# Kernel optimization log

Hardware: AMD Instinct MI355X
Metric: run time of the kernel (lower is better)

## Reference

```python
import jax, jax.numpy as jnp
import numpy as np

D = 4096  # domain size of every variable X, Y, Z, W


def setup_inputs() -> dict:
    key = jax.random.key(0)
    ks = jax.random.split(key, 7)
    theta0 = jax.random.normal(ks[0], (D, D), dtype=jnp.float32)  # clique (X, Y)
    theta1 = jax.random.normal(ks[1], (D, D), dtype=jnp.float32)  # clique (Y, Z)
    theta2 = jax.random.normal(ks[2], (D, D), dtype=jnp.float32)  # clique (Z, W)
    ops = {f"op{i}": jax.random.randint(ks[3 + i], (2, D), 0, D, dtype=jnp.int32)
           for i in range(4)}
    return {"theta0": theta0, "theta1": theta1, "theta2": theta2, **ops}


def _remap(proc, op, dom):
    # torch: zeros(dom).index_add_(0, op[1], proc[op[0]])
    return jnp.zeros((dom,), proc.dtype).at[op[1]].add(proc[op[0]])


def reference(theta0, theta1, theta2, op0, op1, op2, op3):
    dom = theta0.shape[0]
    # m0: clique0 -> clique1 (forward): sum over X (dim 0), remap Y, broadcast over Z
    m0 = _remap(jnp.sum(theta0, axis=0), op0, dom)
    theta1 = theta1 + m0[:, None]          # reshape_dims [True, False]
    # m1: clique1 -> clique2 (forward): sum over Y (dim 0), remap Z
    m1 = _remap(jnp.sum(theta1, axis=0), op1, dom)
    theta2 = theta2 + m1[:, None]
    # m2: clique2 -> clique1 (backward): sum over W (dim 1), subtract stored fwd msg m1
    m2 = _remap(jnp.sum(theta2, axis=1) - m1, op2, dom)
    theta1 = theta1 + m2[None, :]          # reshape_dims [False, True]
    # m3: clique1 -> clique0 (backward): sum over Z (dim 1), subtract stored fwd msg m0
    m3 = _remap(jnp.sum(theta1, axis=1) - m0, op3, dom)
    theta0 = theta0 + m3[None, :]
    return (theta0, theta1, theta2)
```

## Files before the change

### kernel.cpp

```cpp
#include <hip/hip_runtime.h>

#define D 4096

typedef float fx4 __attribute__((ext_vector_type(4)));

#define CS0 0
#define CS1 D
#define RS1 (2 * D)
#define RS2 (3 * D)
#define M0O (4 * D)
#define M1O (5 * D)
#define M2O (6 * D)
#define M3O (7 * D)
#define S2S (8 * D)

__global__ void __launch_bounds__(256) colsum_kernel(
        const float* __restrict__ t0, const float* __restrict__ t1,
        float* __restrict__ ws) {
    int b = blockIdx.x;
    const float* A = (b < 256) ? t0 : t1;
    float* out = ws + ((b < 256) ? CS0 : CS1);
    int lb = b & 255;
    int c4 = (lb & 3) * 256 + threadIdx.x;
    int r0 = (lb >> 2) * 64;
    const fx4* A4 = (const fx4*)A;
    fx4 s = (fx4){0.f, 0.f, 0.f, 0.f};
    #pragma unroll 8
    for (int r = 0; r < 64; ++r)
        s += A4[(size_t)(r0 + r) * (D / 4) + c4];
    atomicAdd(&out[c4 * 4 + 0], s.x);
    atomicAdd(&out[c4 * 4 + 1], s.y);
    atomicAdd(&out[c4 * 4 + 2], s.z);
    atomicAdd(&out[c4 * 4 + 3], s.w);
}


__device__ __forceinline__ float block_sum_1024(float v, float* red) {
    #pragma unroll
    for (int o = 32; o > 0; o >>= 1) v += __shfl_down(v, o);
    int lane = threadIdx.x & 63, wid = threadIdx.x >> 6;
    if (lane == 0) red[wid] = v;
    __syncthreads();
    if (threadIdx.x == 0) {
        float t = 0.f;
        #pragma unroll
        for (int w = 0; w < 16; ++w) t += red[w];
        red[0] = t;
    }
    __syncthreads();
    float r = red[0];
    __syncthreads();
    return r;
}

__global__ void __launch_bounds__(1024) msgsA_kernel(
        float* __restrict__ ws, const int* __restrict__ op0,
        const int* __restrict__ op1) {
    __shared__ float m0[D], m1[D];
    __shared__ float red[16];
    int tid = threadIdx.x;

    int s0[4], d0[4], s1[4], d1[4];
    #pragma unroll
    for (int k = 0; k < 4; ++k) {
        int i = tid + k * 1024;
        s0[k] = op0[i]; d0[k] = op0[D + i];
        s1[k] = op1[i]; d1[k] = op1[D + i];
    }
    float g0[4], g1[4];
    #pragma unroll
    for (int k = 0; k < 4; ++k) {
        g0[k] = ws[CS0 + s0[k]];
        g1[k] = ws[CS1 + s1[k]];
    }
    #pragma unroll
    for (int k = 0; k < 4; ++k) {
        int i = tid + k * 1024;
        m0[i] = 0.f; m1[i] = 0.f;
    }
    __syncthreads();
    #pragma unroll
    for (int k = 0; k < 4; ++k) atomicAdd(&m0[d0[k]], g0[k]);
    __syncthreads();
    float p = 0.f;
    #pragma unroll
    for (int k = 0; k < 4; ++k) p += m0[tid + k * 1024];
    float S0 = block_sum_1024(p, red);
    #pragma unroll
    for (int k = 0; k < 4; ++k) atomicAdd(&m1[d1[k]], g1[k] + S0);
    __syncthreads();
    #pragma unroll
    for (int k = 0; k < 4; ++k) {
        int i = tid + k * 1024;
        ws[M0O + i] = m0[i];
        ws[M1O + i] = m1[i];
    }
}

__global__ void __launch_bounds__(1024) msgsB_kernel(
        float* __restrict__ ws, const int* __restrict__ op2) {
    __shared__ float m2[D];
    __shared__ float red[16];
    int tid = threadIdx.x;

    int s2[4], d2[4];
    #pragma unroll
    for (int k = 0; k < 4; ++k) {
        int i = tid + k * 1024;
        s2[k] = op2[i]; d2[k] = op2[D + i];
    }
    float g2[4];
    #pragma unroll
    for (int k = 0; k < 4; ++k)
        g2[k] = ws[RS2 + s2[k]] + 4095.0f * ws[M1O + s2[k]];
    #pragma unroll
    for (int k = 0; k < 4; ++k) m2[tid + k * 1024] = 0.f;
    __syncthreads();
    #pragma unroll
    for (int k = 0; k < 4; ++k) atomicAdd(&m2[d2[k]], g2[k]);
    __syncthreads();
    float p = 0.f;
    #pragma unroll
    for (int k = 0; k < 4; ++k) p += m2[tid + k * 1024];
    float S2 = block_sum_1024(p, red);
    #pragma unroll
    for (int k = 0; k < 4; ++k) {
        int i = tid + k * 1024;
        ws[M2O + i] = m2[i];
    }
    if (tid == 0) ws[S2S] = S2;
}

__global__ void __launch_bounds__(1024) msgsC_kernel(
        float* __restrict__ ws, const int* __restrict__ op3) {
    __shared__ float m3[D];
    int tid = threadIdx.x;

    int s3[4], d3[4];
    #pragma unroll
    for (int k = 0; k < 4; ++k) {
        int i = tid + k * 1024;
        s3[k] = op3[i]; d3[k] = op3[D + i];
    }
    float S2 = ws[S2S];
    float g3[4];
    #pragma unroll
    for (int k = 0; k < 4; ++k)
        g3[k] = ws[RS1 + s3[k]] + 4095.0f * ws[M0O + s3[k]] + S2;
    #pragma unroll
    for (int k = 0; k < 4; ++k) m3[tid + k * 1024] = 0.f;
    __syncthreads();
    #pragma unroll
    for (int k = 0; k < 4; ++k) atomicAdd(&m3[d3[k]], g3[k]);
    __syncthreads();
    #pragma unroll
    for (int k = 0; k < 4; ++k) {
        int i = tid + k * 1024;
        ws[M3O + i] = m3[i];
    }
}


__device__ __forceinline__ void row_reduce_store(float s, float* dst) {
    __shared__ float red[4];
    #pragma unroll
    for (int o = 32; o > 0; o >>= 1) s += __shfl_down(s, o);
    int lane = threadIdx.x & 63, wid = threadIdx.x >> 6;
    if (lane == 0) red[wid] = s;
    __syncthreads();
    if (threadIdx.x == 0) *dst = (red[0] + red[1]) + (red[2] + red[3]);
}

__global__ void __launch_bounds__(256) applyT2_kernel(
        const float* __restrict__ t2, float* __restrict__ ws,
        float* __restrict__ out2) {
    int row = blockIdx.x;
    size_t base = (size_t)row * D;
    const fx4* src = (const fx4*)(t2 + base);
    fx4* dst = (fx4*)(out2 + base);
    float rr = ws[M1O + row];

    fx4 v[4];
    float s = 0.f;
    #pragma unroll
    for (int k = 0; k < 4; ++k) {
        v[k] = src[threadIdx.x + 256 * k];
        s += (v[k].x + v[k].y) + (v[k].z + v[k].w);
    }
    #pragma unroll
    for (int k = 0; k < 4; ++k)
        __builtin_nontemporal_store(v[k] + rr, &dst[threadIdx.x + 256 * k]);
    row_reduce_store(s, ws + RS2 + row);
}

__global__ void __launch_bounds__(256) applyT1_kernel(
        const float* __restrict__ t1, float* __restrict__ ws,
        float* __restrict__ out1) {
    int row = blockIdx.x;
    size_t base = (size_t)row * D;
    const fx4* src = (const fx4*)(t1 + base);
    const fx4* c4 = (const fx4*)(ws + M2O);
    fx4* dst = (fx4*)(out1 + base);
    float rr = ws[M0O + row];

    fx4 v[4], c[4];
    float s = 0.f;
    #pragma unroll
    for (int k = 0; k < 4; ++k) {
        v[k] = src[threadIdx.x + 256 * k];
        c[k] = c4[threadIdx.x + 256 * k];
        s += (v[k].x + v[k].y) + (v[k].z + v[k].w);
    }
    #pragma unroll
    for (int k = 0; k < 4; ++k)
        __builtin_nontemporal_store(v[k] + c[k] + rr,
                                    &dst[threadIdx.x + 256 * k]);
    row_reduce_store(s, ws + RS1 + row);
}

__global__ void __launch_bounds__(256) applyT0_kernel(
        const float* __restrict__ t0, const float* __restrict__ ws,
        float* __restrict__ out0) {
    int row = blockIdx.x;
    size_t base = (size_t)row * D;
    const fx4* src = (const fx4*)(t0 + base);
    const fx4* c4 = (const fx4*)(ws + M3O);
    fx4* dst = (fx4*)(out0 + base);

    #pragma unroll
    for (int k = 0; k < 4; ++k) {
        fx4 r = src[threadIdx.x + 256 * k] + c4[threadIdx.x + 256 * k];
        __builtin_nontemporal_store(r, &dst[threadIdx.x + 256 * k]);
    }
}

extern "C" void kernel_launch(void* const* d_in, const int* in_sizes, int n_in,
                              void* d_out, int out_size, void* d_ws, size_t ws_size,
                              hipStream_t stream) {
    const float* t0 = (const float*)d_in[0];
    const float* t1 = (const float*)d_in[1];
    const float* t2 = (const float*)d_in[2];
    const int* op0 = (const int*)d_in[3];
    const int* op1 = (const int*)d_in[4];
    const int* op2 = (const int*)d_in[5];
    const int* op3 = (const int*)d_in[6];
    float* out = (float*)d_out;
    float* ws = (float*)d_ws;

    hipMemsetAsync(ws, 0, 2 * D * sizeof(float), stream);

    colsum_kernel<<<512, 256, 0, stream>>>(t0, t1, ws);
    msgsA_kernel<<<1, 1024, 0, stream>>>(ws, op0, op1);
    applyT2_kernel<<<D, 256, 0, stream>>>(t2, ws, out + 2 * (size_t)D * D);
    msgsB_kernel<<<1, 1024, 0, stream>>>(ws, op2);
    applyT1_kernel<<<D, 256, 0, stream>>>(t1, ws, out + 1 * (size_t)D * D);
    msgsC_kernel<<<1, 1024, 0, stream>>>(ws, op3);
    applyT0_kernel<<<D, 256, 0, stream>>>(t0, ws, out + 0 * (size_t)D * D);
}
```

Before: 135.0 us.

## Fuse single-block message kernels into preceding kernels via last-block-done counters

Folds each single-block message computation (msgsA/B/C) into the tail of the preceding grid-wide kernel. A global atomic counter elects the last finishing block, which then performs the scatter-add remap. This removes three kernel launches and their serialization gaps. In exchange, the tail message work runs on 256 threads instead of 1024, each block adds an atomic counter increment, and the row sums now use atomicAdd into a zeroed workspace whose memset grows.

```diff
diff --git a/kernel.cpp b/kernel.cpp
--- a/kernel.cpp
+++ b/kernel.cpp
@@ -8,214 +8,225 @@
 #define CS1 D
 #define RS1 (2 * D)
 #define RS2 (3 * D)
-#define M0O (4 * D)
-#define M1O (5 * D)
-#define M2O (6 * D)
-#define M3O (7 * D)
-#define S2S (8 * D)
-
-__global__ void __launch_bounds__(256) colsum_kernel(
-        const float* __restrict__ t0, const float* __restrict__ t1,
-        float* __restrict__ ws) {
-    int b = blockIdx.x;
-    const float* A = (b < 256) ? t0 : t1;
-    float* out = ws + ((b < 256) ? CS0 : CS1);
-    int lb = b & 255;
-    int c4 = (lb & 3) * 256 + threadIdx.x;
-    int r0 = (lb >> 2) * 64;
-    const fx4* A4 = (const fx4*)A;
-    fx4 s = (fx4){0.f, 0.f, 0.f, 0.f};
-    #pragma unroll 8
-    for (int r = 0; r < 64; ++r)
-        s += A4[(size_t)(r0 + r) * (D / 4) + c4];
-    atomicAdd(&out[c4 * 4 + 0], s.x);
-    atomicAdd(&out[c4 * 4 + 1], s.y);
-    atomicAdd(&out[c4 * 4 + 2], s.z);
-    atomicAdd(&out[c4 * 4 + 3], s.w);
-}
-
-
-__device__ __forceinline__ float block_sum_1024(float v, float* red) {
+#define CNTA (4 * D)
+#define CNTB (4 * D + 1)
+#define CNTC (4 * D + 2)
+#define M0O (4 * D + 16)
+#define M1O (5 * D + 16)
+#define M2O (6 * D + 16)
+#define M3O (7 * D + 16)
+#define S2S (8 * D + 16)
+
+__device__ __forceinline__ float block_sum_256(float v, float* red) {
     #pragma unroll
     for (int o = 32; o > 0; o >>= 1) v += __shfl_down(v, o);
     int lane = threadIdx.x & 63, wid = threadIdx.x >> 6;
     if (lane == 0) red[wid] = v;
     __syncthreads();
-    if (threadIdx.x == 0) {
-        float t = 0.f;
-        #pragma unroll
-        for (int w = 0; w < 16; ++w) t += red[w];
-        red[0] = t;
-    }
+    if (threadIdx.x == 0) red[0] = (red[0] + red[1]) + (red[2] + red[3]);
     __syncthreads();
     float r = red[0];
     __syncthreads();
     return r;
 }
 
-__global__ void __launch_bounds__(1024) msgsA_kernel(
-        float* __restrict__ ws, const int* __restrict__ op0,
-        const int* __restrict__ op1) {
+__global__ void __launch_bounds__(256) colsum_msgsA_kernel(
+        const float* __restrict__ t0, const float* __restrict__ t1,
+        float* __restrict__ ws,
+        const int* __restrict__ op0, const int* __restrict__ op1) {
+    int b = blockIdx.x, tid = threadIdx.x;
+    {
+        const float* A = (b < 256) ? t0 : t1;
+        float* outp = ws + ((b < 256) ? CS0 : CS1);
+        int lb = b & 255;
+        int c4 = (lb & 3) * 256 + tid;
+        int r0 = (lb >> 2) * 64;
+        const fx4* A4 = (const fx4*)A;
+        fx4 s = (fx4){0.f, 0.f, 0.f, 0.f};
+        #pragma unroll 8
+        for (int r = 0; r < 64; ++r)
+            s += A4[(size_t)(r0 + r) * (D / 4) + c4];
+        atomicAdd(&outp[c4 * 4 + 0], s.x);
+        atomicAdd(&outp[c4 * 4 + 1], s.y);
+        atomicAdd(&outp[c4 * 4 + 2], s.z);
+        atomicAdd(&outp[c4 * 4 + 3], s.w);
+    }
+    __syncthreads();
+    __shared__ unsigned int lastflag;
+    if (tid == 0)
+        lastflag = (atomicAdd((unsigned int*)(ws + CNTA), 1u) == 511u);
+    __syncthreads();
+    if (!lastflag) return;
+    __threadfence();
+
     __shared__ float m0[D], m1[D];
-    __shared__ float red[16];
-    int tid = threadIdx.x;
-
-    int s0[4], d0[4], s1[4], d1[4];
-    #pragma unroll
-    for (int k = 0; k < 4; ++k) {
-        int i = tid + k * 1024;
-        s0[k] = op0[i]; d0[k] = op0[D + i];
-        s1[k] = op1[i]; d1[k] = op1[D + i];
-    }
-    float g0[4], g1[4];
-    #pragma unroll
-    for (int k = 0; k < 4; ++k) {
-        g0[k] = ws[CS0 + s0[k]];
-        g1[k] = ws[CS1 + s1[k]];
-    }
-    #pragma unroll
-    for (int k = 0; k < 4; ++k) {
-        int i = tid + k * 1024;
-        m0[i] = 0.f; m1[i] = 0.f;
-    }
-    __syncthreads();
-    #pragma unroll
-    for (int k = 0; k < 4; ++k) atomicAdd(&m0[d0[k]], g0[k]);
+    __shared__ float red[4];
+    #pragma unroll
+    for (int k = 0; k < 16; ++k) {
+        m0[tid + 256 * k] = 0.f; m1[tid + 256 * k] = 0.f;
+    }
+    __syncthreads();
+    #pragma unroll
+    for (int c = 0; c < 2; ++c) {
+        int sx[8], dx[8]; float g[8];
+        #pragma unroll
+        for (int j = 0; j < 8; ++j) {
+            int i = tid + (c * 8 + j) * 256;
+            sx[j] = op0[i]; dx[j] = op0[D + i];
+        }
+        #pragma unroll
+        for (int j = 0; j < 8; ++j) g[j] = ws[CS0 + sx[j]];
+        #pragma unroll
+        for (int j = 0; j < 8; ++j) atomicAdd(&m0[dx[j]], g[j]);
+    }
     __syncthreads();
     float p = 0.f;
     #pragma unroll
-    for (int k = 0; k < 4; ++k) p += m0[tid + k * 1024];
-    float S0 = block_sum_1024(p, red);
-    #pragma unroll
-    for (int k = 0; k < 4; ++k) atomicAdd(&m1[d1[k]], g1[k] + S0);
-    __syncthreads();
-    #pragma unroll
-    for (int k = 0; k < 4; ++k) {
-        int i = tid + k * 1024;
-        ws[M0O + i] = m0[i];
-        ws[M1O + i] = m1[i];
-    }
-}
-
-__global__ void __launch_bounds__(1024) msgsB_kernel(
-        float* __restrict__ ws, const int* __restrict__ op2) {
+    for (int k = 0; k < 16; ++k) p += m0[tid + 256 * k];
+    float S0 = block_sum_256(p, red);
+    #pragma unroll
+    for (int c = 0; c < 2; ++c) {
+        int sx[8], dx[8]; float g[8];
+        #pragma unroll
+        for (int j = 0; j < 8; ++j) {
+            int i = tid + (c * 8 + j) * 256;
+            sx[j] = op1[i]; dx[j] = op1[D + i];
+        }
+        #pragma unroll
+        for (int j = 0; j < 8; ++j) g[j] = ws[CS1 + sx[j]];
+        #pragma unroll
+        for (int j = 0; j < 8; ++j) atomicAdd(&m1[dx[j]], g[j] + S0);
+    }
+    __syncthreads();
+    #pragma unroll
+    for (int k = 0; k < 16; ++k) {
+        ws[M0O + tid + 256 * k] = m0[tid + 256 * k];
+        ws[M1O + tid + 256 * k] = m1[tid + 256 * k];
+    }
+}
+
+__global__ void __launch_bounds__(256) applyT2_msgsB_kernel(
+        const float* __restrict__ t2, float* __restrict__ ws,
+        float* __restrict__ out2, const int* __restrict__ op2) {
+    int row = blockIdx.x, tid = threadIdx.x;
+    __shared__ float red[4];
+    {
+        size_t base = (size_t)row * D;
+        const fx4* src = (const fx4*)(t2 + base);
+        fx4* dst = (fx4*)(out2 + base);
+        float rr = ws[M1O + row];
+        fx4 v[4]; float s = 0.f;
+        #pragma unroll
+        for (int k = 0; k < 4; ++k) {
+            v[k] = src[tid + 256 * k];
+            s += (v[k].x + v[k].y) + (v[k].z + v[k].w);
+        }
+        #pragma unroll
+        for (int k = 0; k < 4; ++k)
+            __builtin_nontemporal_store(v[k] + rr, &dst[tid + 256 * k]);
+        #pragma unroll
+        for (int o = 32; o > 0; o >>= 1) s += __shfl_down(s, o);
+        int lane = tid & 63, wid = tid >> 6;
+        if (lane == 0) red[wid] = s;
+        __syncthreads();
+        if (tid == 0)
+            atomicAdd(&ws[RS2 + row], (red[0] + red[1]) + (red[2] + red[3]));
+    }
+    __syncthreads();
+    __shared__ unsigned int lastflag;
+    if (tid == 0)
+        lastflag = (atomicAdd((unsigned int*)(ws + CNTB), 1u) == (unsigned)(D - 1));
+    __syncthreads();
+    if (!lastflag) return;
+    __threadfence();
+
     __shared__ float m2[D];
-    __shared__ float red[16];
-    int tid = threadIdx.x;
-
-    int s2[4], d2[4];
-    #pragma unroll
-    for (int k = 0; k < 4; ++k) {
-        int i = tid + k * 1024;
-        s2[k] = op2[i]; d2[k] = op2[D + i];
-    }
-    float g2[4];
-    #pragma unroll
-    for (int k = 0; k < 4; ++k)
-        g2[k] = ws[RS2 + s2[k]] + 4095.0f * ws[M1O + s2[k]];
-    #pragma unroll
-    for (int k = 0; k < 4; ++k) m2[tid + k * 1024] = 0.f;
-    __syncthreads();
-    #pragma unroll
-    for (int k = 0; k < 4; ++k) atomicAdd(&m2[d2[k]], g2[k]);
+    #pragma unroll
+    for (int k = 0; k < 16; ++k) m2[tid + 256 * k] = 0.f;
+    __syncthreads();
+    #pragma unroll
+    for (int c = 0; c < 2; ++c) {
+        int sx[8], dx[8]; float g[8];
+        #pragma unroll
+        for (int j = 0; j < 8; ++j) {
+            int i = tid + (c * 8 + j) * 256;
+            sx[j] = op2[i]; dx[j] = op2[D + i];
+        }
+        #pragma unroll
+        for (int j = 0; j < 8; ++j)
+            g[j] = ws[RS2 + sx[j]] + 4095.0f * ws[M1O + sx[j]];
+        #pragma unroll
+        for (int j = 0; j < 8; ++j) atomicAdd(&m2[dx[j]], g[j]);
+    }
     __syncthreads();
     float p = 0.f;
     #pragma unroll
-    for (int k = 0; k < 4; ++k) p += m2[tid + k * 1024];
-    float S2 = block_sum_1024(p, red);
-    #pragma unroll
-    for (int k = 0; k < 4; ++k) {
-        int i = tid + k * 1024;
-        ws[M2O + i] = m2[i];
-    }
+    for (int k = 0; k < 16; ++k) p += m2[tid + 256 * k];
+    float S2 = block_sum_256(p, red);
+    #pragma unroll
+    for (int k = 0; k < 16; ++k) ws[M2O + tid + 256 * k] = m2[tid + 256 * k];
     if (tid == 0) ws[S2S] = S2;
 }
 
-__global__ void __launch_bounds__(1024) msgsC_kernel(
-        float* __restrict__ ws, const int* __restrict__ op3) {
+__global__ void __launch_bounds__(256) applyT1_msgsC_kernel(
+        const float* __restrict__ t1, float* __restrict__ ws,
+        float* __restrict__ out1, const int* __restrict__ op3) {
+    int row = blockIdx.x, tid = threadIdx.x;
+    __shared__ float red[4];
+    {
+        size_t base = (size_t)row * D;
+        const fx4* src = (const fx4*)(t1 + base);
+        const fx4* c4 = (const fx4*)(ws + M2O);
+        fx4* dst = (fx4*)(out1 + base);
+        float rr = ws[M0O + row];
+        fx4 v[4], c[4]; float s = 0.f;
+        #pragma unroll
+        for (int k = 0; k < 4; ++k) {
+            v[k] = src[tid + 256 * k];
+            c[k] = c4[tid + 256 * k];
+            s += (v[k].x + v[k].y) + (v[k].z + v[k].w);
+        }
+        #pragma unroll
+        for (int k = 0; k < 4; ++k)
+            __builtin_nontemporal_store(v[k] + c[k] + rr, &dst[tid + 256 * k]);
+        #pragma unroll
+        for (int o = 32; o > 0; o >>= 1) s += __shfl_down(s, o);
+        int lane = tid & 63, wid = tid >> 6;
+        if (lane == 0) red[wid] = s;
+        __syncthreads();
+        if (tid == 0)
+            atomicAdd(&ws[RS1 + row], (red[0] + red[1]) + (red[2] + red[3]));
+    }
+    __syncthreads();
+    __shared__ unsigned int lastflag;
+    if (tid == 0)
+        lastflag = (atomicAdd((unsigned int*)(ws + CNTC), 1u) == (unsigned)(D - 1));
+    __syncthreads();
+    if (!lastflag) return;
+    __threadfence();
+
     __shared__ float m3[D];
-    int tid = threadIdx.x;
-
-    int s3[4], d3[4];
-    #pragma unroll
-    for (int k = 0; k < 4; ++k) {
-        int i = tid + k * 1024;
-        s3[k] = op3[i]; d3[k] = op3[D + i];
-    }
     float S2 = ws[S2S];
-    float g3[4];
-    #pragma unroll
-    for (int k = 0; k < 4; ++k)
-        g3[k] = ws[RS1 + s3[k]] + 4095.0f * ws[M0O + s3[k]] + S2;
-    #pragma unroll
-    for (int k = 0; k < 4; ++k) m3[tid + k * 1024] = 0.f;
-    __syncthreads();
-    #pragma unroll
-    for (int k = 0; k < 4; ++k) atomicAdd(&m3[d3[k]], g3[k]);
-    __syncthreads();
-    #pragma unroll
-    for (int k = 0; k < 4; ++k) {
-        int i = tid + k * 1024;
-        ws[M3O + i] = m3[i];
-    }
-}
-
-
-__device__ __forceinline__ void row_reduce_store(float s, float* dst) {
-    __shared__ float red[4];
-    #pragma unroll
-    for (int o = 32; o > 0; o >>= 1) s += __shfl_down(s, o);
-    int lane = threadIdx.x & 63, wid = threadIdx.x >> 6;
-    if (lane == 0) red[wid] = s;
-    __syncthreads();
-    if (threadIdx.x == 0) *dst = (red[0] + red[1]) + (red[2] + red[3]);
-}
-
-__global__ void __launch_bounds__(256) applyT2_kernel(
-        const float* __restrict__ t2, float* __restrict__ ws,
-        float* __restrict__ out2) {
-    int row = blockIdx.x;
-    size_t base = (size_t)row * D;
-    const fx4* src = (const fx4*)(t2 + base);
-    fx4* dst = (fx4*)(out2 + base);
-    float rr = ws[M1O + row];
-
-    fx4 v[4];
-    float s = 0.f;
-    #pragma unroll
-    for (int k = 0; k < 4; ++k) {
-        v[k] = src[threadIdx.x + 256 * k];
-        s += (v[k].x + v[k].y) + (v[k].z + v[k].w);
-    }
-    #pragma unroll
-    for (int k = 0; k < 4; ++k)
-        __builtin_nontemporal_store(v[k] + rr, &dst[threadIdx.x + 256 * k]);
-    row_reduce_store(s, ws + RS2 + row);
-}
-
-__global__ void __launch_bounds__(256) applyT1_kernel(
-        const float* __restrict__ t1, float* __restrict__ ws,
-        float* __restrict__ out1) {
-    int row = blockIdx.x;
-    size_t base = (size_t)row * D;
-    const fx4* src = (const fx4*)(t1 + base);
-    const fx4* c4 = (const fx4*)(ws + M2O);
-    fx4* dst = (fx4*)(out1 + base);
-    float rr = ws[M0O + row];
-
-    fx4 v[4], c[4];
-    float s = 0.f;
-    #pragma unroll
-    for (int k = 0; k < 4; ++k) {
-        v[k] = src[threadIdx.x + 256 * k];
-        c[k] = c4[threadIdx.x + 256 * k];
-        s += (v[k].x + v[k].y) + (v[k].z + v[k].w);
-    }
-    #pragma unroll
-    for (int k = 0; k < 4; ++k)
-        __builtin_nontemporal_store(v[k] + c[k] + rr,
-                                    &dst[threadIdx.x + 256 * k]);
-    row_reduce_store(s, ws + RS1 + row);
+    #pragma unroll
+    for (int k = 0; k < 16; ++k) m3[tid + 256 * k] = 0.f;
+    __syncthreads();
+    #pragma unroll
+    for (int c = 0; c < 2; ++c) {
+        int sx[8], dx[8]; float g[8];
+        #pragma unroll
+        for (int j = 0; j < 8; ++j) {
+            int i = tid + (c * 8 + j) * 256;
+            sx[j] = op3[i]; dx[j] = op3[D + i];
+        }
+        #pragma unroll
+        for (int j = 0; j < 8; ++j)
+            g[j] = ws[RS1 + sx[j]] + 4095.0f * ws[M0O + sx[j]] + S2;
+        #pragma unroll
+        for (int j = 0; j < 8; ++j) atomicAdd(&m3[dx[j]], g[j]);
+    }
+    __syncthreads();
+    #pragma unroll
+    for (int k = 0; k < 16; ++k) ws[M3O + tid + 256 * k] = m3[tid + 256 * k];
 }
 
 __global__ void __launch_bounds__(256) applyT0_kernel(
@@ -226,7 +237,6 @@
     const fx4* src = (const fx4*)(t0 + base);
     const fx4* c4 = (const fx4*)(ws + M3O);
     fx4* dst = (fx4*)(out0 + base);
-
     #pragma unroll
     for (int k = 0; k < 4; ++k) {
         fx4 r = src[threadIdx.x + 256 * k] + c4[threadIdx.x + 256 * k];
@@ -247,13 +257,10 @@
     float* out = (float*)d_out;
     float* ws = (float*)d_ws;
 
-    hipMemsetAsync(ws, 0, 2 * D * sizeof(float), stream);
-
-    colsum_kernel<<<512, 256, 0, stream>>>(t0, t1, ws);
-    msgsA_kernel<<<1, 1024, 0, stream>>>(ws, op0, op1);
-    applyT2_kernel<<<D, 256, 0, stream>>>(t2, ws, out + 2 * (size_t)D * D);
-    msgsB_kernel<<<1, 1024, 0, stream>>>(ws, op2);
-    applyT1_kernel<<<D, 256, 0, stream>>>(t1, ws, out + 1 * (size_t)D * D);
-    msgsC_kernel<<<1, 1024, 0, stream>>>(ws, op3);
+    hipMemsetAsync(ws, 0, (4 * D + 16) * sizeof(float), stream);
+
+    colsum_msgsA_kernel<<<512, 256, 0, stream>>>(t0, t1, ws, op0, op1);
+    applyT2_msgsB_kernel<<<D, 256, 0, stream>>>(t2, ws, out + 2 * (size_t)D * D, op2);
+    applyT1_msgsC_kernel<<<D, 256, 0, stream>>>(t1, ws, out + 1 * (size_t)D * D, op3);
     applyT0_kernel<<<D, 256, 0, stream>>>(t0, ws, out + 0 * (size_t)D * D);
 }
```

Measured after the change: 191.0 us. 1.42x slower.

## Precompute theta1 row sums in reduce pass and merge backward message kernels

Applied to the files above, without the earlier changes.

Row sums of the original theta1 are now computed in the first reduction kernel, using 1024 extra blocks with one wave per row, instead of in applyT1. The m2 and m3 message computations are merged into one single-block kernel, which removes one launch and one serial dependency. applyT1 becomes a pure elementwise add with no reduction. The cost is a second read of theta1 in the first pass, about 64 MB of extra traffic, in exchange for one fewer serialized single-block kernel launch.

```diff
diff --git a/kernel.cpp b/kernel.cpp
--- a/kernel.cpp
+++ b/kernel.cpp
@@ -12,26 +12,41 @@
 #define M1O (5 * D)
 #define M2O (6 * D)
 #define M3O (7 * D)
-#define S2S (8 * D)
-
-__global__ void __launch_bounds__(256) colsum_kernel(
+
+__global__ void __launch_bounds__(256) reduce_kernel(
         const float* __restrict__ t0, const float* __restrict__ t1,
         float* __restrict__ ws) {
     int b = blockIdx.x;
-    const float* A = (b < 256) ? t0 : t1;
-    float* out = ws + ((b < 256) ? CS0 : CS1);
-    int lb = b & 255;
-    int c4 = (lb & 3) * 256 + threadIdx.x;
-    int r0 = (lb >> 2) * 64;
-    const fx4* A4 = (const fx4*)A;
-    fx4 s = (fx4){0.f, 0.f, 0.f, 0.f};
-    #pragma unroll 8
-    for (int r = 0; r < 64; ++r)
-        s += A4[(size_t)(r0 + r) * (D / 4) + c4];
-    atomicAdd(&out[c4 * 4 + 0], s.x);
-    atomicAdd(&out[c4 * 4 + 1], s.y);
-    atomicAdd(&out[c4 * 4 + 2], s.z);
-    atomicAdd(&out[c4 * 4 + 3], s.w);
+    if (b < 512) {
+        const float* A = (b < 256) ? t0 : t1;
+        float* out = ws + ((b < 256) ? CS0 : CS1);
+        int lb = b & 255;
+        int c4 = (lb & 3) * 256 + threadIdx.x;
+        int r0 = (lb >> 2) * 64;
+        const fx4* A4 = (const fx4*)A;
+        fx4 s = (fx4){0.f, 0.f, 0.f, 0.f};
+        #pragma unroll 8
+        for (int r = 0; r < 64; ++r)
+            s += A4[(size_t)(r0 + r) * (D / 4) + c4];
+        atomicAdd(&out[c4 * 4 + 0], s.x);
+        atomicAdd(&out[c4 * 4 + 1], s.y);
+        atomicAdd(&out[c4 * 4 + 2], s.z);
+        atomicAdd(&out[c4 * 4 + 3], s.w);
+    } else {
+        int lb = b - 512;
+        int wid = threadIdx.x >> 6, lane = threadIdx.x & 63;
+        int row = lb * 4 + wid;
+        const fx4* R = (const fx4*)(t1 + (size_t)row * D);
+        float s = 0.f;
+        #pragma unroll
+        for (int j = 0; j < 16; ++j) {
+            fx4 v = R[lane + 64 * j];
+            s += (v.x + v.y) + (v.z + v.w);
+        }
+        #pragma unroll
+        for (int o = 32; o > 0; o >>= 1) s += __shfl_down(s, o);
+        if (lane == 0) ws[RS1 + row] = s;
+    }
 }
 
 
@@ -97,24 +112,31 @@
     }
 }
 
-__global__ void __launch_bounds__(1024) msgsB_kernel(
-        float* __restrict__ ws, const int* __restrict__ op2) {
-    __shared__ float m2[D];
+__global__ void __launch_bounds__(1024) msgsBC_kernel(
+        float* __restrict__ ws, const int* __restrict__ op2,
+        const int* __restrict__ op3) {
+    __shared__ float m2[D], m3[D];
     __shared__ float red[16];
     int tid = threadIdx.x;
 
-    int s2[4], d2[4];
+    int s2[4], d2[4], s3[4], d3[4];
     #pragma unroll
     for (int k = 0; k < 4; ++k) {
         int i = tid + k * 1024;
         s2[k] = op2[i]; d2[k] = op2[D + i];
-    }
-    float g2[4];
-    #pragma unroll
-    for (int k = 0; k < 4; ++k)
-        g2[k] = ws[RS2 + s2[k]] + 4095.0f * ws[M1O + s2[k]];
-    #pragma unroll
-    for (int k = 0; k < 4; ++k) m2[tid + k * 1024] = 0.f;
+        s3[k] = op3[i]; d3[k] = op3[D + i];
+    }
+    float g2[4], g3p[4];
+    #pragma unroll
+    for (int k = 0; k < 4; ++k) {
+        g2[k]  = ws[RS2 + s2[k]] + 4095.0f * ws[M1O + s2[k]];
+        g3p[k] = ws[RS1 + s3[k]] + 4095.0f * ws[M0O + s3[k]];
+    }
+    #pragma unroll
+    for (int k = 0; k < 4; ++k) {
+        int i = tid + k * 1024;
+        m2[i] = 0.f; m3[i] = 0.f;
+    }
     __syncthreads();
     #pragma unroll
     for (int k = 0; k < 4; ++k) atomicAdd(&m2[d2[k]], g2[k]);
@@ -124,38 +146,12 @@
     for (int k = 0; k < 4; ++k) p += m2[tid + k * 1024];
     float S2 = block_sum_1024(p, red);
     #pragma unroll
+    for (int k = 0; k < 4; ++k) atomicAdd(&m3[d3[k]], g3p[k] + S2);
+    __syncthreads();
+    #pragma unroll
     for (int k = 0; k < 4; ++k) {
         int i = tid + k * 1024;
         ws[M2O + i] = m2[i];
-    }
-    if (tid == 0) ws[S2S] = S2;
-}
-
-__global__ void __launch_bounds__(1024) msgsC_kernel(
-        float* __restrict__ ws, const int* __restrict__ op3) {
-    __shared__ float m3[D];
-    int tid = threadIdx.x;
-
-    int s3[4], d3[4];
-    #pragma unroll
-    for (int k = 0; k < 4; ++k) {
-        int i = tid + k * 1024;
-        s3[k] = op3[i]; d3[k] = op3[D + i];
-    }
-    float S2 = ws[S2S];
-    float g3[4];
-    #pragma unroll
-    for (int k = 0; k < 4; ++k)
-        g3[k] = ws[RS1 + s3[k]] + 4095.0f * ws[M0O + s3[k]] + S2;
-    #pragma unroll
-    for (int k = 0; k < 4; ++k) m3[tid + k * 1024] = 0.f;
-    __syncthreads();
-    #pragma unroll
-    for (int k = 0; k < 4; ++k) atomicAdd(&m3[d3[k]], g3[k]);
-    __syncthreads();
-    #pragma unroll
-    for (int k = 0; k < 4; ++k) {
-        int i = tid + k * 1024;
         ws[M3O + i] = m3[i];
     }
 }
@@ -194,7 +190,7 @@
 }
 
 __global__ void __launch_bounds__(256) applyT1_kernel(
-        const float* __restrict__ t1, float* __restrict__ ws,
+        const float* __restrict__ t1, const float* __restrict__ ws,
         float* __restrict__ out1) {
     int row = blockIdx.x;
     size_t base = (size_t)row * D;
@@ -203,19 +199,11 @@
     fx4* dst = (fx4*)(out1 + base);
     float rr = ws[M0O + row];
 
-    fx4 v[4], c[4];
-    float s = 0.f;
-    #pragma unroll
-    for (int k = 0; k < 4; ++k) {
-        v[k] = src[threadIdx.x + 256 * k];
-        c[k] = c4[threadIdx.x + 256 * k];
-        s += (v[k].x + v[k].y) + (v[k].z + v[k].w);
-    }
-    #pragma unroll
-    for (int k = 0; k < 4; ++k)
-        __builtin_nontemporal_store(v[k] + c[k] + rr,
-                                    &dst[threadIdx.x + 256 * k]);
-    row_reduce_store(s, ws + RS1 + row);
+    #pragma unroll
+    for (int k = 0; k < 4; ++k) {
+        fx4 r = src[threadIdx.x + 256 * k] + c4[threadIdx.x + 256 * k] + rr;
+        __builtin_nontemporal_store(r, &dst[threadIdx.x + 256 * k]);
+    }
 }
 
 __global__ void __launch_bounds__(256) applyT0_kernel(
@@ -249,11 +237,10 @@
 
     hipMemsetAsync(ws, 0, 2 * D * sizeof(float), stream);
 
-    colsum_kernel<<<512, 256, 0, stream>>>(t0, t1, ws);
+    reduce_kernel<<<1536, 256, 0, stream>>>(t0, t1, ws);
     msgsA_kernel<<<1, 1024, 0, stream>>>(ws, op0, op1);
     applyT2_kernel<<<D, 256, 0, stream>>>(t2, ws, out + 2 * (size_t)D * D);
-    msgsB_kernel<<<1, 1024, 0, stream>>>(ws, op2);
+    msgsBC_kernel<<<1, 1024, 0, stream>>>(ws, op2, op3);
     applyT1_kernel<<<D, 256, 0, stream>>>(t1, ws, out + 1 * (size_t)D * D);
-    msgsC_kernel<<<1, 1024, 0, stream>>>(ws, op3);
     applyT0_kernel<<<D, 256, 0, stream>>>(t0, ws, out + 0 * (size_t)D * D);
 }
```

Result: slower. 140.6 us (+4.1%).
